# Performance work log

Hardware: AMD Instinct MI355X
Metric: run time of the kernel (lower is better)

## Reference

```python
import jax, jax.numpy as jnp
import numpy as np

N, D, S, C = 2048, 1024, 49, 1000


def setup_inputs() -> dict:
    key = jax.random.key(0)
    k1, k2, k3 = jax.random.split(key, 3)
    x = jax.random.normal(k1, (N, D, S), dtype=jnp.float32)
    mu = jax.random.normal(k2, (C, D), dtype=jnp.float32)
    # precision = inverse covariance -> symmetric PSD; build a well-conditioned one
    R = jax.random.normal(k3, (D, D), dtype=jnp.float32)
    precision = (R @ R.T) / D + jnp.eye(D, dtype=jnp.float32)
    return {"x": x, "mu": mu, "precision": precision}


def reference(x, mu, precision):
    # z: [N, D] global-average-pooled features (z.view(N, D, -1).mean(2))
    z = jnp.mean(x, axis=2)
    # score[n, c] = -0.5 * (z_n - mu_c) @ P @ (z_n - mu_c)
    # Expanded to avoid materializing [N, C, D]:
    #   zPz - z P mu - mu P z + mu P mu   (no symmetry assumption on P)
    zP = z @ precision                      # [N, D]
    zPt = z @ precision.T                   # [N, D]
    qz = jnp.sum(zP * z, axis=1)            # [N]   diag(z P z^T)
    cross1 = zP @ mu.T                      # [N, C] z P mu
    cross2 = zPt @ mu.T                     # [N, C] mu P z
    qmu = jnp.einsum('cd,de,ce->c', mu, precision, mu)  # [C]
    score = -0.5 * (qz[:, None] - cross1 - cross2 + qmu[None, :])
    return score
```

## Files before the change

### kernel.cpp

```cpp
#include <hip/hip_runtime.h>
#include <hip/hip_bf16.h>

typedef unsigned short u16;
typedef __bf16 bf16x8 __attribute__((ext_vector_type(8)));
typedef float f32x4 __attribute__((ext_vector_type(4)));

typedef const __attribute__((address_space(1))) void gv_t;
typedef __attribute__((address_space(3))) void lv_t;

#define NN 2048
#define DD 1024
#define SS 49
#define CC 1000
#define CP 1024

#define BK 64
#define KK DD
#define NT (KK / BK)

__device__ inline u16 f2bf(float f) {
    __hip_bfloat16 h = __float2bfloat16(f);
    union { __hip_bfloat16 h; u16 u; } cv; cv.h = h; return cv.u;
}

__device__ __forceinline__ void gemm64_core(const u16* __restrict__ A,
                                            const u16* __restrict__ Bt,
                                            int m0, int n0, char* smem,
                                            f32x4 acc[2][2], int tid) {
    char* As = smem;
    char* Bs = smem + 16384;
    const int lane = tid & 63;
    const int wr = (tid >> 6) >> 1, wc = (tid >> 6) & 1;
    const int r16 = lane & 15, hk = lane >> 4;
    const char* Ab = (const char*)A;
    const char* Bb = (const char*)Bt;

    auto stage = [&](int buf, int k0) {
        #pragma unroll
        for (int j = 0; j < 2; j++) {
            const int c = j * 256 + tid;
            const int row = c >> 3, slot = c & 7;
            const int goff = ((slot ^ (row & 7)) << 4);
            __builtin_amdgcn_global_load_lds(
                (gv_t*)(Ab + ((size_t)(m0 + row) * KK + k0) * 2 + goff),
                (lv_t*)(As + buf * 8192 + c * 16), 16, 0, 0);
            __builtin_amdgcn_global_load_lds(
                (gv_t*)(Bb + ((size_t)(n0 + row) * KK + k0) * 2 + goff),
                (lv_t*)(Bs + buf * 8192 + c * 16), 16, 0, 0);
        }
    };

    stage(0, 0);
    __syncthreads();
    int cur = 0;
    for (int t = 0; t < NT; ++t) {
        if (t + 1 < NT) stage(cur ^ 1, (t + 1) * BK);
        bf16x8 a[2][2], b[2][2];
        #pragma unroll
        for (int mi = 0; mi < 2; mi++) {
            const int row = wr * 32 + mi * 16 + r16;
            #pragma unroll
            for (int kk2 = 0; kk2 < 2; kk2++) {
                const int g = kk2 * 4 + hk;
                a[mi][kk2] = *(const bf16x8*)(As + cur * 8192 + row * 128 + ((g ^ (row & 7)) << 4));
            }
        }
        #pragma unroll
        for (int ni = 0; ni < 2; ni++) {
            const int row = wc * 32 + ni * 16 + r16;
            #pragma unroll
            for (int kk2 = 0; kk2 < 2; kk2++) {
                const int g = kk2 * 4 + hk;
                b[ni][kk2] = *(const bf16x8*)(Bs + cur * 8192 + row * 128 + ((g ^ (row & 7)) << 4));
            }
        }
        #pragma unroll
        for (int kk2 = 0; kk2 < 2; kk2++)
            #pragma unroll
            for (int mi = 0; mi < 2; mi++)
                #pragma unroll
                for (int ni = 0; ni < 2; ni++)
                    acc[mi][ni] = __builtin_amdgcn_mfma_f32_16x16x32_bf16(
                        a[mi][kk2], b[ni][kk2], acc[mi][ni], 0, 0, 0);
        __syncthreads();
        cur ^= 1;
    }
}

__global__ __launch_bounds__(256) void prep_k(const float* __restrict__ P,
                                              const float* __restrict__ mu,
                                              u16* __restrict__ q,
                                              u16* __restrict__ mu_bf,
                                              float* __restrict__ qzh,
                                              float* __restrict__ qmuh) {
    __shared__ float t1[64][65];
    __shared__ float t2[64][65];
    const int tid = threadIdx.x, bid = blockIdx.x;
    const int br = bid >> 4, bc = bid & 15;
    const int br64 = br * 64, bc64 = bc * 64;

    #pragma unroll
    for (int it = 0; it < 16; it++) {
        const int idx = it * 256 + tid;
        const int row = idx >> 6, col = idx & 63;
        t1[row][col] = P[(size_t)(br64 + row) * DD + bc64 + col];
        t2[row][col] = P[(size_t)(bc64 + row) * DD + br64 + col];
    }
    __syncthreads();
    #pragma unroll
    for (int it = 0; it < 16; it++) {
        const int idx = it * 256 + tid;
        const int row = idx >> 6, col = idx & 63;
        q[(size_t)(br64 + row) * DD + bc64 + col] = f2bf(t1[row][col] + t2[col][row]);
    }

    const size_t base = (size_t)bid * 4096;
    #pragma unroll
    for (int it = 0; it < 16; it++) {
        const size_t j = base + it * 256 + tid;
        const int r = (int)(j >> 10);
        mu_bf[j] = f2bf(r < CC ? mu[j] : 0.f);
    }
    const int g = bid * 256 + tid;
    if (g < NN) qzh[g]  = 0.f;
    if (g < CP) qmuh[g] = 0.f;
}

__global__ __launch_bounds__(256) void pool_muq_k(const float* __restrict__ x,
                                                  const u16* __restrict__ q,
                                                  const u16* __restrict__ mu_bf,
                                                  const float* __restrict__ mu,
                                                  u16* __restrict__ b_bf,
                                                  float* __restrict__ qmuh,
                                                  float* __restrict__ zf,
                                                  u16* __restrict__ zb) {
    __shared__ char smem[50176];
    const int tid = threadIdx.x;
    const int bid = blockIdx.x;

    if (bid >= 256) {
        const int u = bid - 256;
        float* lds = (float*)smem;
        const size_t base = (size_t)u * (256 * SS);
        const float4* src = (const float4*)(x + base);
        float4* dst = (float4*)lds;
        #pragma unroll
        for (int i = 0; i < 13; i++) {
            int idx = i * 256 + tid;
            if (idx < (256 * SS) / 4) dst[idx] = src[idx];
        }
        __syncthreads();
        const float* r = lds + tid * SS;
        float s = 0.f;
        #pragma unroll
        for (int j = 0; j < SS; j++) s += r[j];
        s *= (1.f / 49.f);
        size_t o = (size_t)u * 256 + tid;
        zf[o] = s;
        zb[o] = f2bf(s);
        return;
    }

    const int m0 = (bid >> 4) * 64, n0 = (bid & 15) * 64;
    f32x4 acc[2][2] = {};
    gemm64_core(mu_bf, q, m0, n0, smem, acc, tid);

    const int lane = tid & 63;
    const int wr = (tid >> 6) >> 1, wc = (tid >> 6) & 1;
    const int cr = (lane >> 4) * 4, cc2 = lane & 15;
    #pragma unroll
    for (int mi = 0; mi < 2; mi++) {
        const int gr0 = m0 + wr * 32 + mi * 16 + cr;
        #pragma unroll
        for (int r = 0; r < 4; r++) {
            const int row = gr0 + r;
            float v = 0.f;
            #pragma unroll
            for (int ni = 0; ni < 2; ni++) {
                const int gc = n0 + wc * 32 + ni * 16 + cc2;
                float av = acc[mi][ni][r];
                float sv = (row < CC) ? mu[(size_t)row * DD + gc] : 0.f;
                v += av * sv;
                b_bf[(size_t)row * DD + gc] = f2bf(av);
            }
            #pragma unroll
            for (int m = 1; m < 16; m <<= 1) v += __shfl_xor(v, m);
            if (cc2 == 0) atomicAdd(qmuh + row, 0.25f * v);
        }
    }
}

__global__ __launch_bounds__(256) void zgemm_k(const u16* __restrict__ z_bf,
                                               const u16* __restrict__ q,
                                               const u16* __restrict__ b_bf,
                                               const float* __restrict__ zf,
                                               float* __restrict__ qzh,
                                               const float* __restrict__ qmuh,
                                               float* __restrict__ out) {
    __shared__ char smem[32768];
    const int tid = threadIdx.x;
    const int bid = blockIdx.x;
    const int lane = tid & 63;
    const int wr = (tid >> 6) >> 1, wc = (tid >> 6) & 1;
    const int cr = (lane >> 4) * 4, cc2 = lane & 15;

    if (bid < 512) {
        const int m0 = (bid >> 4) * 64, n0 = (bid & 15) * 64;
        f32x4 acc[2][2] = {};
        gemm64_core(z_bf, q, m0, n0, smem, acc, tid);
        #pragma unroll
        for (int mi = 0; mi < 2; mi++) {
            const int gr0 = m0 + wr * 32 + mi * 16 + cr;
            #pragma unroll
            for (int r = 0; r < 4; r++) {
                const int row = gr0 + r;
                float v = 0.f;
                #pragma unroll
                for (int ni = 0; ni < 2; ni++) {
                    const int gc = n0 + wc * 32 + ni * 16 + cc2;
                    v += acc[mi][ni][r] * zf[(size_t)row * DD + gc];
                }
                #pragma unroll
                for (int m = 1; m < 16; m <<= 1) v += __shfl_xor(v, m);
                if (cc2 == 0) atomicAdd(qzh + row, 0.25f * v);
            }
        }
    } else {
        const int i = bid - 512;
        const int m0 = (i >> 4) * 64, n0 = (i & 15) * 64;
        f32x4 acc[2][2] = {};
        gemm64_core(z_bf, b_bf, m0, n0, smem, acc, tid);
        #pragma unroll
        for (int mi = 0; mi < 2; mi++) {
            #pragma unroll
            for (int ni = 0; ni < 2; ni++) {
                const int gr = m0 + wr * 32 + mi * 16 + cr;
                const int gc = n0 + wc * 32 + ni * 16 + cc2;
                if (gc < CC) {
                    const float qm = qmuh[gc];
                    #pragma unroll
                    for (int r = 0; r < 4; r++)
                        out[(size_t)(gr + r) * CC + gc] =
                            0.5f * acc[mi][ni][r] - qm;
                }
            }
        }
    }
}

__global__ __launch_bounds__(256) void fixup_k(float* __restrict__ out,
                                               const float* __restrict__ qzh) {
    const int n = blockIdx.x, tid = threadIdx.x;
    if (tid >= 250) return;
    const float qz = qzh[n];
    float4* p = (float4*)(out + (size_t)n * CC + tid * 4);
    float4 v = *p;
    v.x -= qz; v.y -= qz; v.z -= qz; v.w -= qz;
    *p = v;
}

extern "C" void kernel_launch(void* const* d_in, const int* in_sizes, int n_in,
                              void* d_out, int out_size, void* d_ws, size_t ws_size,
                              hipStream_t stream) {
    const float* x  = (const float*)d_in[0];
    const float* mu = (const float*)d_in[1];
    const float* P  = (const float*)d_in[2];
    float* out = (float*)d_out;

    char* w = (char*)d_ws;
    u16*   q_bf  = (u16*)w;   w += (size_t)DD * DD * 2;
    u16*   mu_bf = (u16*)w;   w += (size_t)CP * DD * 2;
    u16*   b_bf  = (u16*)w;   w += (size_t)CP * DD * 2;
    u16*   z_bf  = (u16*)w;   w += (size_t)NN * DD * 2;
    float* zf    = (float*)w; w += (size_t)NN * DD * 4;
    float* qzh   = (float*)w; w += (size_t)NN * 4;
    float* qmuh  = (float*)w;

    prep_k<<<256, 256, 0, stream>>>(P, mu, q_bf, mu_bf, qzh, qmuh);
    pool_muq_k<<<256 + (NN * DD) / 256, 256, 0, stream>>>(
        x, q_bf, mu_bf, mu, b_bf, qmuh, zf, z_bf);
    zgemm_k<<<1024, 256, 0, stream>>>(z_bf, q_bf, b_bf, zf, qzh, qmuh, out);
    fixup_k<<<NN, 256, 0, stream>>>(out, qzh);
}
```

Baseline: 120.0 us.

## Fuse z@Q and z@B GEMMs into one kernel sharing the A tile

Replaces the two block-split GEMMs, each with its own launch half, by a single kernel that stages one z tile plus two B tiles (Q and the mu-derived matrix) per K step and runs both MFMA chains on the shared A fragments. This halves the loads of z tiles and the block count from 1024 to 512, at the cost of more LDS (48KB) and twice the accumulator registers per block, which may lower occupancy. Both epilogues (qz atomic reduction and score write) now run in the same block.

Result: no change. 120.6 us (+0.5%).

```diff
diff --git a/kernel.cpp b/kernel.cpp
--- a/kernel.cpp
+++ b/kernel.cpp
@@ -190,59 +190,117 @@
     }
 }
 
-__global__ __launch_bounds__(256) void zgemm_k(const u16* __restrict__ z_bf,
-                                               const u16* __restrict__ q,
-                                               const u16* __restrict__ b_bf,
-                                               const float* __restrict__ zf,
-                                               float* __restrict__ qzh,
-                                               const float* __restrict__ qmuh,
-                                               float* __restrict__ out) {
-    __shared__ char smem[32768];
-    const int tid = threadIdx.x;
-    const int bid = blockIdx.x;
+__global__ __launch_bounds__(256) void zscore_k(const u16* __restrict__ z_bf,
+                                                const u16* __restrict__ q,
+                                                const u16* __restrict__ b_bf,
+                                                const float* __restrict__ zf,
+                                                float* __restrict__ qzh,
+                                                const float* __restrict__ qmuh,
+                                                float* __restrict__ out) {
+    __shared__ char smem[49152];
+    const int tid = threadIdx.x, bid = blockIdx.x;
+    const int m0 = (bid >> 4) * 64, n0 = (bid & 15) * 64;
     const int lane = tid & 63;
     const int wr = (tid >> 6) >> 1, wc = (tid >> 6) & 1;
-    const int cr = (lane >> 4) * 4, cc2 = lane & 15;
-
-    if (bid < 512) {
-        const int m0 = (bid >> 4) * 64, n0 = (bid & 15) * 64;
-        f32x4 acc[2][2] = {};
-        gemm64_core(z_bf, q, m0, n0, smem, acc, tid);
+    const int r16 = lane & 15, hk = lane >> 4;
+    char* As = smem;
+    char* Bq = smem + 16384;
+    char* Bb = smem + 32768;
+    const char* Ap = (const char*)z_bf;
+    const char* Qp = (const char*)q;
+    const char* Bp = (const char*)b_bf;
+
+    f32x4 accS[2][2] = {};
+    f32x4 accZ[2][2] = {};
+
+    auto stage = [&](int buf, int k0) {
+        #pragma unroll
+        for (int j = 0; j < 2; j++) {
+            const int c = j * 256 + tid;
+            const int row = c >> 3, slot = c & 7;
+            const int goff = ((slot ^ (row & 7)) << 4);
+            const size_t ao = ((size_t)(m0 + row) * KK + k0) * 2 + goff;
+            const size_t bo = ((size_t)(n0 + row) * KK + k0) * 2 + goff;
+            __builtin_amdgcn_global_load_lds((gv_t*)(Ap + ao),
+                (lv_t*)(As + buf * 8192 + c * 16), 16, 0, 0);
+            __builtin_amdgcn_global_load_lds((gv_t*)(Qp + bo),
+                (lv_t*)(Bq + buf * 8192 + c * 16), 16, 0, 0);
+            __builtin_amdgcn_global_load_lds((gv_t*)(Bp + bo),
+                (lv_t*)(Bb + buf * 8192 + c * 16), 16, 0, 0);
+        }
+    };
+
+    stage(0, 0);
+    __syncthreads();
+    int cur = 0;
+    for (int t = 0; t < NT; ++t) {
+        if (t + 1 < NT) stage(cur ^ 1, (t + 1) * BK);
+        bf16x8 a[2][2], bq[2][2], bb[2][2];
         #pragma unroll
         for (int mi = 0; mi < 2; mi++) {
-            const int gr0 = m0 + wr * 32 + mi * 16 + cr;
-            #pragma unroll
-            for (int r = 0; r < 4; r++) {
-                const int row = gr0 + r;
-                float v = 0.f;
+            const int row = wr * 32 + mi * 16 + r16;
+            #pragma unroll
+            for (int kk2 = 0; kk2 < 2; kk2++) {
+                const int g = kk2 * 4 + hk;
+                a[mi][kk2] = *(const bf16x8*)(As + cur * 8192 + row * 128 + ((g ^ (row & 7)) << 4));
+            }
+        }
+        #pragma unroll
+        for (int ni = 0; ni < 2; ni++) {
+            const int row = wc * 32 + ni * 16 + r16;
+            #pragma unroll
+            for (int kk2 = 0; kk2 < 2; kk2++) {
+                const int g = kk2 * 4 + hk;
+                const int off = row * 128 + ((g ^ (row & 7)) << 4);
+                bq[ni][kk2] = *(const bf16x8*)(Bq + cur * 8192 + off);
+                bb[ni][kk2] = *(const bf16x8*)(Bb + cur * 8192 + off);
+            }
+        }
+        #pragma unroll
+        for (int kk2 = 0; kk2 < 2; kk2++)
+            #pragma unroll
+            for (int mi = 0; mi < 2; mi++)
                 #pragma unroll
                 for (int ni = 0; ni < 2; ni++) {
-                    const int gc = n0 + wc * 32 + ni * 16 + cc2;
-                    v += acc[mi][ni][r] * zf[(size_t)row * DD + gc];
+                    accS[mi][ni] = __builtin_amdgcn_mfma_f32_16x16x32_bf16(
+                        a[mi][kk2], bb[ni][kk2], accS[mi][ni], 0, 0, 0);
+                    accZ[mi][ni] = __builtin_amdgcn_mfma_f32_16x16x32_bf16(
+                        a[mi][kk2], bq[ni][kk2], accZ[mi][ni], 0, 0, 0);
                 }
+        __syncthreads();
+        cur ^= 1;
+    }
+
+    const int cr = hk * 4, cc2 = r16;
+    #pragma unroll
+    for (int mi = 0; mi < 2; mi++) {
+        const int gr0 = m0 + wr * 32 + mi * 16 + cr;
+        #pragma unroll
+        for (int r = 0; r < 4; r++) {
+            const int row = gr0 + r;
+            float v = 0.f;
+            #pragma unroll
+            for (int ni = 0; ni < 2; ni++) {
+                const int gc = n0 + wc * 32 + ni * 16 + cc2;
+                v += accZ[mi][ni][r] * zf[(size_t)row * DD + gc];
+            }
+            #pragma unroll
+            for (int m = 1; m < 16; m <<= 1) v += __shfl_xor(v, m);
+            if (cc2 == 0) atomicAdd(qzh + row, 0.25f * v);
+        }
+    }
+    #pragma unroll
+    for (int mi = 0; mi < 2; mi++) {
+        #pragma unroll
+        for (int ni = 0; ni < 2; ni++) {
+            const int gr = m0 + wr * 32 + mi * 16 + cr;
+            const int gc = n0 + wc * 32 + ni * 16 + cc2;
+            if (gc < CC) {
+                const float qm = qmuh[gc];
                 #pragma unroll
-                for (int m = 1; m < 16; m <<= 1) v += __shfl_xor(v, m);
-                if (cc2 == 0) atomicAdd(qzh + row, 0.25f * v);
-            }
-        }
-    } else {
-        const int i = bid - 512;
-        const int m0 = (i >> 4) * 64, n0 = (i & 15) * 64;
-        f32x4 acc[2][2] = {};
-        gemm64_core(z_bf, b_bf, m0, n0, smem, acc, tid);
-        #pragma unroll
-        for (int mi = 0; mi < 2; mi++) {
-            #pragma unroll
-            for (int ni = 0; ni < 2; ni++) {
-                const int gr = m0 + wr * 32 + mi * 16 + cr;
-                const int gc = n0 + wc * 32 + ni * 16 + cc2;
-                if (gc < CC) {
-                    const float qm = qmuh[gc];
-                    #pragma unroll
-                    for (int r = 0; r < 4; r++)
-                        out[(size_t)(gr + r) * CC + gc] =
-                            0.5f * acc[mi][ni][r] - qm;
-                }
+                for (int r = 0; r < 4; r++)
+                    out[(size_t)(gr + r) * CC + gc] =
+                        0.5f * accS[mi][ni][r] - qm;
             }
         }
     }
@@ -279,6 +337,6 @@
     prep_k<<<256, 256, 0, stream>>>(P, mu, q_bf, mu_bf, qzh, qmuh);
     pool_muq_k<<<256 + (NN * DD) / 256, 256, 0, stream>>>(
         x, q_bf, mu_bf, mu, b_bf, qmuh, zf, z_bf);
-    zgemm_k<<<1024, 256, 0, stream>>>(z_bf, q_bf, b_bf, zf, qzh, qmuh, out);
+    zscore_k<<<512, 256, 0, stream>>>(z_bf, q_bf, b_bf, zf, qzh, qmuh, out);
     fixup_k<<<NN, 256, 0, stream>>>(out, qzh);
 }
```
